# Optimization experiments

Measured on AMD Instinct MI355X. Metric: run time of the kernel, lower is better.

The kernel has to match this reference:

```python
import jax, jax.numpy as jnp
import numpy as np

B, S, D = 16, 1024, 768          # batch, seq_len, in_features
NS, MAXW = 256, 8                # num_spans, max span width (fixed for jit)
V, C = 128, 6                    # num_vertexes, max corefs per vertex
R = 512                          # num_max_rels_per_example
REL, HID, DIS = 97, 384, 20      # relation_num, hidden_dim, dis_size
NEG = -1e30


def setup_inputs() -> dict:
    key = jax.random.key(0)
    ks = jax.random.split(key, 14)
    sentence_repr = jax.random.normal(ks[0], (B, S, D), jnp.float32)
    starts = jax.random.randint(ks[1], (B, NS), 0, S - MAXW)
    widths = jax.random.randint(ks[2], (B, NS), 0, MAXW)
    entity_span_indices = jnp.stack([starts, starts + widths], axis=-1)  # (B,NS,2), start<=end
    entity_span_indices_mask = jax.random.randint(ks[3], (B, NS), 0, 2)
    vertex_indices = jax.random.randint(ks[4], (B, V, C), 0, NS)
    vertex_indices_mask = jax.random.randint(ks[5], (B, V, C), 0, 2)
    head_tail_indices = jax.random.randint(ks[6], (B, R, 2), 0, V)
    relation_mask = jax.random.randint(ks[7], (B, R), 0, 2)
    dis_h_2_t = jax.random.randint(ks[8], (B, R), 0, 20)
    dis_t_2_h = jax.random.randint(ks[9], (B, R), 0, 20)
    dis_embed = jax.random.normal(ks[10], (20, DIS), jnp.float32) * 0.02
    dis_embed = dis_embed.at[10].set(0.0)  # padding_idx=10
    fin = D + DIS                      # final_in_features with distance
    in_proj = 2 * fin + D              # concat [head+dis, tail+dis, head*tail]
    W1 = jax.random.normal(ks[11], (in_proj, HID), jnp.float32) / np.float32(np.sqrt(in_proj))
    W2 = jax.random.normal(ks[12], (HID, REL), jnp.float32) / np.float32(np.sqrt(HID))
    b2 = jnp.zeros((REL,), jnp.float32)
    return dict(sentence_repr=sentence_repr, entity_span_indices=entity_span_indices,
                entity_span_indices_mask=entity_span_indices_mask,
                vertex_indices=vertex_indices, vertex_indices_mask=vertex_indices_mask,
                head_tail_indices=head_tail_indices, relation_mask=relation_mask,
                dis_h_2_t=dis_h_2_t, dis_t_2_h=dis_t_2_h,
                dis_embed=dis_embed, W1=W1, W2=W2, b2=b2)


def reference(sentence_repr, entity_span_indices, entity_span_indices_mask,
              vertex_indices, vertex_indices_mask, head_tail_indices,
              relation_mask, dis_h_2_t, dis_t_2_h, dis_embed, W1, W2, b2):
    Bx, Sx, Dx = sentence_repr.shape
    # --- SpanExtractor: masked max pooling over tokens in each span [start, end] ---
    starts = entity_span_indices[..., 0]
    ends = entity_span_indices[..., 1]
    pos = starts[..., None] + jnp.arange(MAXW)            # (B,NS,W)
    valid = pos <= ends[..., None]
    posc = jnp.clip(pos, 0, Sx - 1).reshape(Bx, -1)       # (B,NS*W)
    tok = jnp.take_along_axis(sentence_repr, posc[..., None], axis=1)
    tok = tok.reshape(Bx, NS, MAXW, Dx)
    span_emb = jnp.where(valid[..., None], tok, NEG).max(axis=2)   # (B,NS,D)
    # --- coref 'mean' pooling over spans per vertex (batched_index_select) ---
    vidx = vertex_indices.reshape(Bx, -1)
    ve = jnp.take_along_axis(span_emb, vidx[..., None], axis=1).reshape(Bx, V, C, Dx)
    m = vertex_indices_mask.astype(jnp.float32)
    cnt = jnp.maximum(m.sum(axis=2), 1.0)                 # num_corefs clamped >=1
    vertex_emb = (ve * m[..., None]).sum(axis=2) / cnt[..., None]  # (B,V,D)
    # --- head/tail gather ---
    hti = head_tail_indices.reshape(Bx, -1)
    ht = jnp.take_along_axis(vertex_emb, hti[..., None], axis=1).reshape(Bx, R, 2, Dx)
    head_repr = ht[:, :, 0, :]
    tail_repr = ht[:, :, 1, :]
    # (original multiplies by relation_mask and discards the result -> no-op)
    eh = dis_embed[dis_h_2_t]                              # (B,R,DIS)
    et = dis_embed[dis_t_2_h]
    feat = jnp.concatenate([head_repr, eh, tail_repr, et, head_repr * tail_repr], axis=-1)
    # TwoLayerLinear: relu(x @ W1) @ W2 + b2, bias=(False, True)
    predict_re = jax.nn.relu(feat @ W1) @ W2 + b2          # (B,R,REL)
    return predict_re
```

## Files before the change

### kernel.cpp

```cpp
#include <hip/hip_runtime.h>
#include <cstdint>
#include <cstddef>

#define B_    16
#define S_    1024
#define D_    768
#define NS_   256
#define V_    128
#define C_    6
#define R_    512
#define REL_  97
#define HID_  384
#define DIS_  20
#define KD_   768
#define N2P_  128

typedef unsigned short ushort_t;
typedef unsigned int   u32;
typedef short bf16x4 __attribute__((ext_vector_type(4)));
typedef short bf16x8 __attribute__((ext_vector_type(8)));
typedef float f32x4  __attribute__((ext_vector_type(4)));
typedef float f32x16 __attribute__((ext_vector_type(16)));

__device__ __forceinline__ float bf2f(short s) {
    return __uint_as_float(((unsigned int)(unsigned short)s) << 16);
}
__device__ __forceinline__ short f2bf(float x) {
    union { float f; unsigned int u; } c; c.f = x;
    unsigned int r = (c.u + 0x7fffu + ((c.u >> 16) & 1u)) >> 16;
    return (short)(unsigned short)r;
}

typedef const __attribute__((address_space(1))) u32* gas_t;
typedef __attribute__((address_space(3))) u32*       las_t;
__device__ __forceinline__ void dma16(const void* g, void* l) {
    __builtin_amdgcn_global_load_lds((gas_t)g, (las_t)l, 16, 0, 0);
}

__global__ __launch_bounds__(192) void prep_kernel(
    const float* __restrict__ sr, const int* __restrict__ spans,
    const float* __restrict__ W1, const float* __restrict__ W2,
    const float* __restrict__ dis,
    ushort_t* __restrict__ span_emb, ushort_t* __restrict__ W1HT,
    ushort_t* __restrict__ W1P, ushort_t* __restrict__ W2T,
    float* __restrict__ disH, float* __restrict__ disT)
{
    int blk = blockIdx.x;
    int tid = threadIdx.x;
    if (blk < 4096) {
        int bn    = blk;
        int b     = bn >> 8;
        int start = spans[2 * bn];
        int end   = spans[2 * bn + 1];
        int w     = end - start;
        const float* base = sr + ((size_t)b * S_ + start) * D_ + tid * 4;
        f32x4 x[8];
        x[0] = *(const f32x4*)base;
        switch (w) {
        case 7: x[7] = *(const f32x4*)(base + 7 * D_); [[fallthrough]];
        case 6: x[6] = *(const f32x4*)(base + 6 * D_); [[fallthrough]];
        case 5: x[5] = *(const f32x4*)(base + 5 * D_); [[fallthrough]];
        case 4: x[4] = *(const f32x4*)(base + 4 * D_); [[fallthrough]];
        case 3: x[3] = *(const f32x4*)(base + 3 * D_); [[fallthrough]];
        case 2: x[2] = *(const f32x4*)(base + 2 * D_); [[fallthrough]];
        case 1: x[1] = *(const f32x4*)(base + 1 * D_); break;
        default: break;
        }
        f32x4 m = x[0];
#pragma unroll
        for (int j = 1; j < 8; ++j)
            if (j <= w) {
#pragma unroll
                for (int c = 0; c < 4; ++c) m[c] = fmaxf(m[c], x[j][c]);
            }
        bf16x4 o;
#pragma unroll
        for (int c = 0; c < 4; ++c) o[c] = f2bf(m[c]);
        *(bf16x4*)(span_emb + (size_t)bn * D_ + tid * 4) = o;
    } else if (blk < 4480) {
        int flat = (blk - 4096) * 192 + tid;
        int nn   = flat & 63;
        int kg   = (flat >> 6) & 7;
        int itnt = flat >> 9;
        int it   = itnt / 12;
        int nt   = itnt - it * 12;
        bf16x8 p;
#pragma unroll
        for (int j = 0; j < 8; ++j) {
            int k = it * 64 + kg * 8 + j;
            int n = nt * 64 + nn;
            float v = (n < HID_) ? W1[(size_t)k * HID_ + n]
                                 : W1[(size_t)(788 + k) * HID_ + (n - HID_)];
            p[j] = f2bf(v);
        }
        *(bf16x8*)(W1HT + ((size_t)itnt * 8 + kg) * 512 + nn * 8) = p;
    } else if (blk < 4672) {
        int flat = (blk - 4480) * 192 + tid;
        int nn   = flat & 63;
        int kg   = (flat >> 6) & 7;
        int itnt = flat >> 9;
        int it   = itnt / 6;
        int nt   = itnt - it * 6;
        bf16x8 p;
#pragma unroll
        for (int j = 0; j < 8; ++j) {
            int k = it * 64 + kg * 8 + j;
            int n = nt * 64 + nn;
            p[j] = f2bf(W1[(size_t)(1576 + k) * HID_ + n]);
        }
        *(bf16x8*)(W1P + ((size_t)itnt * 8 + kg) * 512 + nn * 8) = p;
    } else if (blk < 4704) {
        int g  = (blk - 4672) * 192 + tid;
        int n  = g / 48;
        int k0 = (g - n * 48) * 8;
        bf16x8 p;
#pragma unroll
        for (int j = 0; j < 8; ++j) {
            float v = (n < REL_) ? W2[(size_t)(k0 + j) * REL_ + n] : 0.f;
            p[j] = f2bf(v);
        }
        *(bf16x8*)(W2T + (size_t)n * HID_ + k0) = p;
    } else {
        int g   = (blk - 4704) * 192 + tid;
        int sel = g >= 7680;
        int gg  = sel ? g - 7680 : g;
        int i   = gg / HID_;
        int n   = gg - i * HID_;
        int rb  = sel ? 1556 : 768;
        float a = 0.f;
#pragma unroll
        for (int j = 0; j < DIS_; ++j)
            a += dis[i * DIS_ + j] * W1[(size_t)(rb + j) * HID_ + n];
        (sel ? disT : disH)[i * HID_ + n] = a;
    }
}

__global__ __launch_bounds__(192) void vertex_kernel(
    const ushort_t* __restrict__ span_emb, const int* __restrict__ vidx,
    const int* __restrict__ vmask, ushort_t* __restrict__ vembB)
{
    int bv = blockIdx.x;
    int b  = bv >> 7;
    const int* vi = vidx  + bv * C_;
    const int* vm = vmask + bv * C_;
    int   idxs[C_];
    float ms[C_];
    float cnt = 0.f;
#pragma unroll
    for (int c = 0; c < C_; ++c) {
        idxs[c] = vi[c];
        ms[c]   = (float)vm[c];
        cnt    += ms[c];
    }
    float inv = 1.f / fmaxf(cnt, 1.f);
    int col = threadIdx.x * 4;
    float s[4] = {0.f, 0.f, 0.f, 0.f};
#pragma unroll
    for (int c = 0; c < C_; ++c) {
        if (ms[c] != 0.f) {
            bf16x4 x = *(const bf16x4*)(span_emb +
                        ((size_t)(b * NS_ + idxs[c])) * D_ + col);
#pragma unroll
            for (int q = 0; q < 4; ++q) s[q] += bf2f(x[q]);
        }
    }
    bf16x4 o;
#pragma unroll
    for (int q = 0; q < 4; ++q) o[q] = f2bf(s[q] * inv);
    *(bf16x4*)(vembB + (size_t)bv * D_ + col) = o;
}

__global__ __launch_bounds__(256, 3) void gemmc_kernel(
    const ushort_t* __restrict__ vembB, const ushort_t* __restrict__ W1HT,
    float* __restrict__ vproj)
{
    __shared__ ushort_t Abuf[2][64][64];
    __shared__ ushort_t Bbuf[2][8][64][8];

    int tid  = threadIdx.x;
    int wv   = tid >> 6;
    int lane = tid & 63;
    int m0   = blockIdx.x * 64;
    int nt   = blockIdx.y;
    int n0   = nt * 64;

    int rr  = lane >> 3;
    int sl  = lane & 7;
    int gsw = (sl - rr) & 7;

    const ushort_t* asrc[2];
#pragma unroll
    for (int gi = 0; gi < 2; ++gi)
        asrc[gi] = vembB + (size_t)(m0 + wv * 16 + gi * 8 + rr) * KD_ + gsw * 8;

    auto stage = [&](int bf, int it) {
#pragma unroll
        for (int gi = 0; gi < 2; ++gi)
            dma16(asrc[gi] + it * 64, &Abuf[bf][wv * 16 + gi * 8][0]);
        const ushort_t* bbase = W1HT + ((size_t)it * 12 + nt) * 4096;
#pragma unroll
        for (int q = 0; q < 2; ++q) {
            int p = wv * 2 + q;
            dma16(bbase + (size_t)p * 512 + lane * 8, &Bbuf[bf][p][0][0]);
        }
    };

    int half = lane >> 5;
    int lrow = lane & 31;
    int wm   = (wv & 1) * 32;
    int wn   = (wv >> 1) * 32;

    f32x16 acc;
#pragma unroll
    for (int r = 0; r < 16; ++r) acc[r] = 0.f;

    stage(0, 0);
    for (int it = 0; it < 12; ++it) {
        int bf = it & 1;
        __syncthreads();
        if (it + 1 < 12) stage(bf ^ 1, it + 1);
#pragma unroll
        for (int s = 0; s < 4; ++s) {
            int kg   = s * 2 + half;
            int slot = ((kg + lrow) & 7) * 8;
            bf16x8 a = *(bf16x8*)&Abuf[bf][wm + lrow][slot];
            bf16x8 b = *(bf16x8*)&Bbuf[bf][kg][wn + lrow][0];
            acc = __builtin_amdgcn_mfma_f32_32x32x16_bf16(a, b, acc, 0, 0, 0);
        }
    }

    int col = n0 + wn + lrow;
#pragma unroll
    for (int r = 0; r < 16; ++r) {
        int row = m0 + wm + (r & 3) + 8 * (r >> 2) + 4 * half;
        vproj[(size_t)row * KD_ + col] = acc[r];
    }
}

__global__ __launch_bounds__(256, 3) void gemmd_kernel(
    const ushort_t* __restrict__ vembB, const int* __restrict__ ht,
    const int* __restrict__ dht, const int* __restrict__ dth,
    const ushort_t* __restrict__ W1P, const float* __restrict__ vproj,
    const float* __restrict__ disH, const float* __restrict__ disT,
    ushort_t* __restrict__ hidden)
{
    __shared__ ushort_t Abuf[2][64][64];
    __shared__ ushort_t Bbuf[2][8][64][8];
    __shared__ int hI[64], tI[64], dhI[64], dtI[64];

    int tid  = threadIdx.x;
    int wv   = tid >> 6;
    int lane = tid & 63;
    int m0   = blockIdx.x * 64;
    int nt   = blockIdx.y;
    int n0   = nt * 64;

    int rr  = lane >> 3;
    int sl  = lane & 7;
    int gsw = (sl - rr) & 7;

    if (tid < 64) {
        int g = m0 + tid;
        int b = g >> 9;
        hI[tid]  = b * V_ + ht[2 * g];
        tI[tid]  = b * V_ + ht[2 * g + 1];
        dhI[tid] = dht[g];
        dtI[tid] = dth[g];
    }

    int hoff[2], toff[2];
#pragma unroll
    for (int gi = 0; gi < 2; ++gi) {
        int g = m0 + wv * 16 + gi * 8 + rr;
        int b = g >> 9;
        hoff[gi] = (b * V_ + ht[2 * g])     * KD_;
        toff[gi] = (b * V_ + ht[2 * g + 1]) * KD_;
    }

    auto stage = [&](int bf, int it) {
        int kk = it * 64 + gsw * 8;
#pragma unroll
        for (int gi = 0; gi < 2; ++gi) {
            bf16x8 h = *(const bf16x8*)(vembB + hoff[gi] + kk);
            bf16x8 t = *(const bf16x8*)(vembB + toff[gi] + kk);
            bf16x8 p;
#pragma unroll
            for (int j = 0; j < 8; ++j) p[j] = f2bf(bf2f(h[j]) * bf2f(t[j]));
            *(bf16x8*)&Abuf[bf][wv * 16 + gi * 8 + rr][sl * 8] = p;
        }
        const ushort_t* bbase = W1P + ((size_t)it * 6 + nt) * 4096;
#pragma unroll
        for (int q = 0; q < 2; ++q) {
            int p = wv * 2 + q;
            dma16(bbase + (size_t)p * 512 + lane * 8, &Bbuf[bf][p][0][0]);
        }
    };

    int half = lane >> 5;
    int lrow = lane & 31;
    int wm   = (wv & 1) * 32;
    int wn   = (wv >> 1) * 32;

    f32x16 acc;
#pragma unroll
    for (int r = 0; r < 16; ++r) acc[r] = 0.f;

    stage(0, 0);
    for (int it = 0; it < 12; ++it) {
        int bf = it & 1;
        __syncthreads();
        if (it + 1 < 12) stage(bf ^ 1, it + 1);
#pragma unroll
        for (int s = 0; s < 4; ++s) {
            int kg   = s * 2 + half;
            int slot = ((kg + lrow) & 7) * 8;
            bf16x8 a = *(bf16x8*)&Abuf[bf][wm + lrow][slot];
            bf16x8 b = *(bf16x8*)&Bbuf[bf][kg][wn + lrow][0];
            acc = __builtin_amdgcn_mfma_f32_32x32x16_bf16(a, b, acc, 0, 0, 0);
        }
    }

    int col = n0 + wn + lrow;
#pragma unroll
    for (int r = 0; r < 16; ++r) {
        int rl = wm + (r & 3) + 8 * (r >> 2) + 4 * half;
        float v = acc[r]
                + vproj[(size_t)hI[rl] * KD_ + col]
                + vproj[(size_t)tI[rl] * KD_ + HID_ + col]
                + disH[dhI[rl] * HID_ + col]
                + disT[dtI[rl] * HID_ + col];
        hidden[(size_t)(m0 + rl) * HID_ + col] = (ushort_t)f2bf(fmaxf(v, 0.f));
    }
}

__global__ __launch_bounds__(256) void gemm2_kernel(
    const ushort_t* __restrict__ hidden, const ushort_t* __restrict__ W2T,
    const float* __restrict__ b2, float* __restrict__ out)
{
    __shared__ ushort_t As[32][72];
    __shared__ ushort_t Bs[128][72];

    int m0  = blockIdx.x * 32;
    int tid = threadIdx.x;

    int arow = tid >> 3;
    int akk  = (tid & 7) * 8;

    bf16x8 pA; bf16x8 pB[4];
    auto loadAB = [&](int k0) {
        pA = *(const bf16x8*)(hidden + (size_t)(m0 + arow) * HID_ + k0 + akk);
#pragma unroll
        for (int e = 0; e < 4; ++e)
            pB[e] = *(const bf16x8*)(W2T + (size_t)(arow + e * 32) * HID_ + k0 + akk);
    };

    int w    = tid >> 6;
    int lane = tid & 63;
    int wm = (w & 1) * 16;
    int wn = (w >> 1) * 64;
    int lr = lane & 15, lq = lane >> 4;

    f32x4 acc[4];
#pragma unroll
    for (int e = 0; e < 4; ++e) acc[e] = (f32x4){0.f, 0.f, 0.f, 0.f};

    loadAB(0);
    for (int k0 = 0; k0 < HID_; k0 += 64) {
        __syncthreads();
        *(bf16x8*)&As[arow][akk] = pA;
#pragma unroll
        for (int e = 0; e < 4; ++e)
            *(bf16x8*)&Bs[arow + e * 32][akk] = pB[e];
        __syncthreads();
        if (k0 + 64 < HID_) loadAB(k0 + 64);
#pragma unroll
        for (int ks = 0; ks < 2; ++ks) {
            int kb = ks * 32 + lq * 8;
            bf16x8 a = *(bf16x8*)&As[wm + lr][kb];
#pragma unroll
            for (int nf = 0; nf < 4; ++nf) {
                bf16x8 bb = *(bf16x8*)&Bs[wn + nf * 16 + lr][kb];
                acc[nf] = __builtin_amdgcn_mfma_f32_16x16x32_bf16(a, bb, acc[nf], 0, 0, 0);
            }
        }
    }

    int grow = m0 + wm + lq * 4;
#pragma unroll
    for (int nf = 0; nf < 4; ++nf) {
        int col = wn + nf * 16 + lr;
        if (col < REL_) {
            float bias = b2[col];
#pragma unroll
            for (int r = 0; r < 4; ++r)
                out[(size_t)(grow + r) * REL_ + col] = acc[nf][r] + bias;
        }
    }
}

extern "C" void kernel_launch(void* const* d_in, const int* in_sizes, int n_in,
                              void* d_out, int out_size, void* d_ws, size_t ws_size,
                              hipStream_t stream)
{
    const float* sr    = (const float*)d_in[0];
    const int*   spans = (const int*)  d_in[1];
    const int*   vidx  = (const int*)  d_in[3];
    const int*   vmask = (const int*)  d_in[4];
    const int*   ht    = (const int*)  d_in[5];
    const int*   dht   = (const int*)  d_in[7];
    const int*   dth   = (const int*)  d_in[8];
    const float* dis   = (const float*)d_in[9];
    const float* W1    = (const float*)d_in[10];
    const float* W2    = (const float*)d_in[11];
    const float* b2    = (const float*)d_in[12];
    float* out = (float*)d_out;

    ushort_t* span_emb = (ushort_t*)d_ws;
    ushort_t* vembB    = span_emb + (size_t)B_ * NS_ * D_;
    ushort_t* W1HT     = vembB + (size_t)B_ * V_ * D_;
    ushort_t* W1P      = W1HT + (size_t)144 * 4096;
    ushort_t* W2T      = W1P + (size_t)72 * 4096;
    ushort_t* hidden   = W2T + (size_t)N2P_ * HID_;
    float* vproj = (float*)(hidden + (size_t)B_ * R_ * HID_);
    float* disH  = vproj + (size_t)B_ * V_ * KD_;
    float* disT  = disH + (size_t)DIS_ * HID_;

    prep_kernel<<<4784, 192, 0, stream>>>(
        sr, spans, W1, W2, dis, span_emb, W1HT, W1P, W2T, disH, disT);
    vertex_kernel<<<B_ * V_, 192, 0, stream>>>(span_emb, vidx, vmask, vembB);

    gemmc_kernel<<<dim3(32, 12), 256, 0, stream>>>(vembB, W1HT, vproj);
    gemmd_kernel<<<dim3(128, 6), 256, 0, stream>>>(
        vembB, ht, dht, dth, W1P, vproj, disH, disT, hidden);

    gemm2_kernel<<<(B_ * R_) / 32, 256, 0, stream>>>(hidden, W2T, b2, out);
}
```

Baseline: 151.6 us.

## Fuse all five stages into one cooperative persistent kernel with grid syncs

Replaces the five separate launches (prep, vertex pooling, two first-layer GEMMs, second GEMM) with one cooperative kernel. The stages are separated by grid.sync() and their work is distributed with grid-stride loops. The aim is to remove per-launch overhead and the drain and fill gaps between kernels. In exchange it needs cooperative launch, caps occupancy via launch bounds, and keeps the old multi-kernel path as a fallback when the stream is being captured or the cooperative launch fails.

```diff
diff --git a/kernel.cpp b/kernel.cpp
--- a/kernel.cpp
+++ b/kernel.cpp
@@ -1,6 +1,9 @@
 #include <hip/hip_runtime.h>
+#include <hip/hip_cooperative_groups.h>
 #include <cstdint>
 #include <cstddef>
+
+namespace cg = cooperative_groups;
 
 #define B_    16
 #define S_    1024
@@ -14,6 +17,8 @@
 #define DIS_  20
 #define KD_   768
 #define N2P_  128
+#define NBLK  768
+#define NTHR  256
 
 typedef unsigned short ushort_t;
 typedef unsigned int   u32;
@@ -35,6 +40,347 @@
 typedef __attribute__((address_space(3))) u32*       las_t;
 __device__ __forceinline__ void dma16(const void* g, void* l) {
     __builtin_amdgcn_global_load_lds((gas_t)g, (las_t)l, 16, 0, 0);
+}
+
+__global__ __launch_bounds__(NTHR, 3) void mega_kernel(
+    const float* __restrict__ sr, const int* __restrict__ spans,
+    const int* __restrict__ vidx, const int* __restrict__ vmask,
+    const int* __restrict__ ht, const int* __restrict__ dht,
+    const int* __restrict__ dth, const float* __restrict__ dis,
+    const float* __restrict__ W1, const float* __restrict__ W2,
+    const float* __restrict__ b2,
+    ushort_t* __restrict__ span_emb, ushort_t* __restrict__ vembB,
+    ushort_t* __restrict__ W1HT, ushort_t* __restrict__ W1P,
+    ushort_t* __restrict__ W2T, float* __restrict__ disH,
+    float* __restrict__ disT, ushort_t* __restrict__ hidden,
+    float* __restrict__ vproj, float* __restrict__ out)
+{
+    cg::grid_group grid = cg::this_grid();
+
+    __shared__ union {
+        struct {
+            ushort_t A[2][64][64];
+            ushort_t Bp[2][8][64][8];
+            int hI[64], tI[64], dhI[64], dtI[64];
+        } cd;
+        struct {
+            ushort_t As[32][72];
+            ushort_t Bs[128][72];
+        } g2;
+    } sm;
+
+    const int tid   = threadIdx.x;
+    const int blk   = blockIdx.x;
+    const int lane  = tid & 63;
+    const int wv    = tid >> 6;
+    const int nblks = gridDim.x;
+    const int gtid  = blk * NTHR + tid;
+    const int nthrd = nblks * NTHR;
+
+    {
+        const int waveid = blk * 4 + wv;
+        const int nwaves = nblks * 4;
+        for (int task = waveid; task < 12288; task += nwaves) {
+            int bn = task & 4095;
+            int q  = task >> 12;
+            int b  = bn >> 8;
+            int start = spans[2 * bn];
+            int end   = spans[2 * bn + 1];
+            int w     = end - start;
+            int col   = q * 256 + lane * 4;
+            const float* base = sr + ((size_t)b * S_ + start) * D_ + col;
+            f32x4 x[8];
+            x[0] = *(const f32x4*)base;
+            switch (w) {
+            case 7: x[7] = *(const f32x4*)(base + 7 * D_); [[fallthrough]];
+            case 6: x[6] = *(const f32x4*)(base + 6 * D_); [[fallthrough]];
+            case 5: x[5] = *(const f32x4*)(base + 5 * D_); [[fallthrough]];
+            case 4: x[4] = *(const f32x4*)(base + 4 * D_); [[fallthrough]];
+            case 3: x[3] = *(const f32x4*)(base + 3 * D_); [[fallthrough]];
+            case 2: x[2] = *(const f32x4*)(base + 2 * D_); [[fallthrough]];
+            case 1: x[1] = *(const f32x4*)(base + 1 * D_); break;
+            default: break;
+            }
+            f32x4 m = x[0];
+#pragma unroll
+            for (int j = 1; j < 8; ++j)
+                if (j <= w) {
+#pragma unroll
+                    for (int c = 0; c < 4; ++c) m[c] = fmaxf(m[c], x[j][c]);
+                }
+            bf16x4 o;
+#pragma unroll
+            for (int c = 0; c < 4; ++c) o[c] = f2bf(m[c]);
+            *(bf16x4*)(span_emb + (size_t)bn * D_ + col) = o;
+        }
+    }
+    for (int g0 = gtid; g0 < 132096; g0 += nthrd) {
+        if (g0 < 73728) {
+            int g = g0;
+            int nn = g & 63, kg = (g >> 6) & 7, itnt = g >> 9;
+            int it = itnt / 12, nt = itnt - it * 12;
+            bf16x8 p;
+#pragma unroll
+            for (int j = 0; j < 8; ++j) {
+                int k = it * 64 + kg * 8 + j;
+                int n = nt * 64 + nn;
+                float v = (n < HID_) ? W1[(size_t)k * HID_ + n]
+                                     : W1[(size_t)(788 + k) * HID_ + (n - HID_)];
+                p[j] = f2bf(v);
+            }
+            *(bf16x8*)(W1HT + ((size_t)itnt * 8 + kg) * 512 + nn * 8) = p;
+        } else if (g0 < 110592) {
+            int g = g0 - 73728;
+            int nn = g & 63, kg = (g >> 6) & 7, itnt = g >> 9;
+            int it = itnt / 6, nt = itnt - it * 6;
+            bf16x8 p;
+#pragma unroll
+            for (int j = 0; j < 8; ++j) {
+                int k = it * 64 + kg * 8 + j;
+                int n = nt * 64 + nn;
+                p[j] = f2bf(W1[(size_t)(1576 + k) * HID_ + n]);
+            }
+            *(bf16x8*)(W1P + ((size_t)itnt * 8 + kg) * 512 + nn * 8) = p;
+        } else if (g0 < 116736) {
+            int g = g0 - 110592;
+            int n = g / 48, k0 = (g - n * 48) * 8;
+            bf16x8 p;
+#pragma unroll
+            for (int j = 0; j < 8; ++j) {
+                float v = (n < REL_) ? W2[(size_t)(k0 + j) * REL_ + n] : 0.f;
+                p[j] = f2bf(v);
+            }
+            *(bf16x8*)(W2T + (size_t)n * HID_ + k0) = p;
+        } else {
+            int g = g0 - 116736;
+            int sel = g >= 7680;
+            int gg = sel ? g - 7680 : g;
+            int i = gg / HID_, n = gg - (gg / HID_) * HID_;
+            int rb = sel ? 1556 : 768;
+            float a = 0.f;
+#pragma unroll
+            for (int j = 0; j < DIS_; ++j)
+                a += dis[i * DIS_ + j] * W1[(size_t)(rb + j) * HID_ + n];
+            (sel ? disT : disH)[i * HID_ + n] = a;
+        }
+    }
+
+    grid.sync();
+
+    for (int task = gtid; task < 393216; task += nthrd) {
+        int bv  = task / 192;
+        int grp = task - bv * 192;
+        int b   = bv >> 7;
+        const int* vi = vidx  + bv * C_;
+        const int* vm = vmask + bv * C_;
+        float cnt = 0.f;
+        float sacc[4] = {0.f, 0.f, 0.f, 0.f};
+        int col = grp * 4;
+#pragma unroll
+        for (int c = 0; c < C_; ++c) {
+            int mc = vm[c];
+            cnt += (float)mc;
+            if (mc) {
+                bf16x4 x = *(const bf16x4*)(span_emb +
+                            ((size_t)(b * NS_ + vi[c])) * D_ + col);
+#pragma unroll
+                for (int q = 0; q < 4; ++q) sacc[q] += bf2f(x[q]);
+            }
+        }
+        float inv = 1.f / fmaxf(cnt, 1.f);
+        bf16x4 o;
+#pragma unroll
+        for (int q = 0; q < 4; ++q) o[q] = f2bf(sacc[q] * inv);
+        *(bf16x4*)(vembB + (size_t)bv * D_ + col) = o;
+    }
+
+    grid.sync();
+
+    for (int bt = blk; bt < 384; bt += nblks) {
+        const int mb = bt & 31, nt = bt >> 5;
+        const int m0 = mb * 64, n0 = nt * 64;
+        const int rr = lane >> 3, sl = lane & 7;
+        const int gsw = (sl - rr) & 7;
+
+        const ushort_t* asrc0 = vembB + (size_t)(m0 + wv * 16 + rr) * KD_ + gsw * 8;
+        const ushort_t* asrc1 = asrc0 + 8 * KD_;
+
+        auto stageC = [&](int bf, int it) {
+            dma16(asrc0 + it * 64, &sm.cd.A[bf][wv * 16][0]);
+            dma16(asrc1 + it * 64, &sm.cd.A[bf][wv * 16 + 8][0]);
+            const ushort_t* bbase = W1HT + ((size_t)it * 12 + nt) * 4096;
+#pragma unroll
+            for (int q = 0; q < 2; ++q) {
+                int p = wv * 2 + q;
+                dma16(bbase + (size_t)p * 512 + lane * 8, &sm.cd.Bp[bf][p][0][0]);
+            }
+        };
+
+        const int half = lane >> 5, lrow = lane & 31;
+        const int wm = (wv & 1) * 32, wn = (wv >> 1) * 32;
+
+        f32x16 acc;
+#pragma unroll
+        for (int r = 0; r < 16; ++r) acc[r] = 0.f;
+
+        stageC(0, 0);
+        for (int it = 0; it < 12; ++it) {
+            int bf = it & 1;
+            __syncthreads();
+            if (it + 1 < 12) stageC(bf ^ 1, it + 1);
+#pragma unroll
+            for (int s = 0; s < 4; ++s) {
+                int kg   = s * 2 + half;
+                int slot = ((kg + lrow) & 7) * 8;
+                bf16x8 a = *(bf16x8*)&sm.cd.A[bf][wm + lrow][slot];
+                bf16x8 b = *(bf16x8*)&sm.cd.Bp[bf][kg][wn + lrow][0];
+                acc = __builtin_amdgcn_mfma_f32_32x32x16_bf16(a, b, acc, 0, 0, 0);
+            }
+        }
+        int col = n0 + wn + lrow;
+#pragma unroll
+        for (int r = 0; r < 16; ++r) {
+            int row = m0 + wm + (r & 3) + 8 * (r >> 2) + 4 * half;
+            vproj[(size_t)row * KD_ + col] = acc[r];
+        }
+    }
+
+    grid.sync();
+
+    for (int bt = blk; bt < 768; bt += nblks) {
+        __syncthreads();
+        const int mb = bt & 127, nt = bt >> 7;
+        const int m0 = mb * 64, n0 = nt * 64;
+        const int rr = lane >> 3, sl = lane & 7;
+        const int gsw = (sl - rr) & 7;
+
+        if (tid < 64) {
+            int g = m0 + tid;
+            int b = g >> 9;
+            sm.cd.hI[tid]  = b * V_ + ht[2 * g];
+            sm.cd.tI[tid]  = b * V_ + ht[2 * g + 1];
+            sm.cd.dhI[tid] = dht[g];
+            sm.cd.dtI[tid] = dth[g];
+        }
+
+        int hoff[2], toff[2];
+#pragma unroll
+        for (int gi = 0; gi < 2; ++gi) {
+            int g = m0 + wv * 16 + gi * 8 + rr;
+            int b = g >> 9;
+            hoff[gi] = (b * V_ + ht[2 * g])     * KD_;
+            toff[gi] = (b * V_ + ht[2 * g + 1]) * KD_;
+        }
+
+        auto stageD = [&](int bf, int it) {
+            int kk = it * 64 + gsw * 8;
+#pragma unroll
+            for (int gi = 0; gi < 2; ++gi) {
+                bf16x8 h = *(const bf16x8*)(vembB + hoff[gi] + kk);
+                bf16x8 t = *(const bf16x8*)(vembB + toff[gi] + kk);
+                bf16x8 p;
+#pragma unroll
+                for (int j = 0; j < 8; ++j) p[j] = f2bf(bf2f(h[j]) * bf2f(t[j]));
+                *(bf16x8*)&sm.cd.A[bf][wv * 16 + gi * 8 + rr][sl * 8] = p;
+            }
+            const ushort_t* bbase = W1P + ((size_t)it * 6 + nt) * 4096;
+#pragma unroll
+            for (int q = 0; q < 2; ++q) {
+                int p = wv * 2 + q;
+                dma16(bbase + (size_t)p * 512 + lane * 8, &sm.cd.Bp[bf][p][0][0]);
+            }
+        };
+
+        const int half = lane >> 5, lrow = lane & 31;
+        const int wm = (wv & 1) * 32, wn = (wv >> 1) * 32;
+
+        f32x16 acc;
+#pragma unroll
+        for (int r = 0; r < 16; ++r) acc[r] = 0.f;
+
+        stageD(0, 0);
+        for (int it = 0; it < 12; ++it) {
+            int bf = it & 1;
+            __syncthreads();
+            if (it + 1 < 12) stageD(bf ^ 1, it + 1);
+#pragma unroll
+            for (int s = 0; s < 4; ++s) {
+                int kg   = s * 2 + half;
+                int slot = ((kg + lrow) & 7) * 8;
+                bf16x8 a = *(bf16x8*)&sm.cd.A[bf][wm + lrow][slot];
+                bf16x8 b = *(bf16x8*)&sm.cd.Bp[bf][kg][wn + lrow][0];
+                acc = __builtin_amdgcn_mfma_f32_32x32x16_bf16(a, b, acc, 0, 0, 0);
+            }
+        }
+
+        int col = n0 + wn + lrow;
+#pragma unroll
+        for (int r = 0; r < 16; ++r) {
+            int rl = wm + (r & 3) + 8 * (r >> 2) + 4 * half;
+            float v = acc[r]
+                    + vproj[(size_t)sm.cd.hI[rl] * KD_ + col]
+                    + vproj[(size_t)sm.cd.tI[rl] * KD_ + HID_ + col]
+                    + disH[sm.cd.dhI[rl] * HID_ + col]
+                    + disT[sm.cd.dtI[rl] * HID_ + col];
+            hidden[(size_t)(m0 + rl) * HID_ + col] = (ushort_t)f2bf(fmaxf(v, 0.f));
+        }
+    }
+
+    grid.sync();
+
+    for (int bt = blk; bt < 256; bt += nblks) {
+        const int m0 = bt * 32;
+        const int arow = tid >> 3;
+        const int akk  = (tid & 7) * 8;
+
+        bf16x8 pA; bf16x8 pB[4];
+        auto loadAB = [&](int k0) {
+            pA = *(const bf16x8*)(hidden + (size_t)(m0 + arow) * HID_ + k0 + akk);
+#pragma unroll
+            for (int e = 0; e < 4; ++e)
+                pB[e] = *(const bf16x8*)(W2T + (size_t)(arow + e * 32) * HID_ + k0 + akk);
+        };
+
+        const int wm = (wv & 1) * 16, wn = (wv >> 1) * 64;
+        const int lr = lane & 15, lq = lane >> 4;
+
+        f32x4 acc[4];
+#pragma unroll
+        for (int e = 0; e < 4; ++e) acc[e] = (f32x4){0.f, 0.f, 0.f, 0.f};
+
+        loadAB(0);
+        for (int k0 = 0; k0 < HID_; k0 += 64) {
+            __syncthreads();
+            *(bf16x8*)&sm.g2.As[arow][akk] = pA;
+#pragma unroll
+            for (int e = 0; e < 4; ++e)
+                *(bf16x8*)&sm.g2.Bs[arow + e * 32][akk] = pB[e];
+            __syncthreads();
+            if (k0 + 64 < HID_) loadAB(k0 + 64);
+#pragma unroll
+            for (int ks = 0; ks < 2; ++ks) {
+                int kb = ks * 32 + lq * 8;
+                bf16x8 a = *(bf16x8*)&sm.g2.As[wm + lr][kb];
+#pragma unroll
+                for (int nf = 0; nf < 4; ++nf) {
+                    bf16x8 bb = *(bf16x8*)&sm.g2.Bs[wn + nf * 16 + lr][kb];
+                    acc[nf] = __builtin_amdgcn_mfma_f32_16x16x32_bf16(a, bb, acc[nf], 0, 0, 0);
+                }
+            }
+        }
+
+        int grow = m0 + wm + lq * 4;
+#pragma unroll
+        for (int nf = 0; nf < 4; ++nf) {
+            int col = wn + nf * 16 + lr;
+            if (col < REL_) {
+                float bias = b2[col];
+#pragma unroll
+                for (int r = 0; r < 4; ++r)
+                    out[(size_t)(grow + r) * REL_ + col] = acc[nf][r] + bias;
+            }
+        }
+    }
 }
 
 __global__ __launch_bounds__(192) void prep_kernel(
@@ -425,13 +771,41 @@
     float* disH  = vproj + (size_t)B_ * V_ * KD_;
     float* disT  = disH + (size_t)DIS_ * HID_;
 
-    prep_kernel<<<4784, 192, 0, stream>>>(
-        sr, spans, W1, W2, dis, span_emb, W1HT, W1P, W2T, disH, disT);
-    vertex_kernel<<<B_ * V_, 192, 0, stream>>>(span_emb, vidx, vmask, vembB);
-
-    gemmc_kernel<<<dim3(32, 12), 256, 0, stream>>>(vembB, W1HT, vproj);
-    gemmd_kernel<<<dim3(128, 6), 256, 0, stream>>>(
-        vembB, ht, dht, dth, W1P, vproj, disH, disT, hidden);
-
-    gemm2_kernel<<<(B_ * R_) / 32, 256, 0, stream>>>(hidden, W2T, b2, out);
-}
+    bool done = false;
+    hipStreamCaptureStatus cs = hipStreamCaptureStatusNone;
+    if (hipStreamIsCapturing(stream, &cs) != hipSuccess)
+        cs = hipStreamCaptureStatusActive;
+    if (cs == hipStreamCaptureStatusNone) {
+        int maxB = 0;
+        if (hipOccupancyMaxActiveBlocksPerMultiprocessor(&maxB, mega_kernel,
+                                                         NTHR, 0) == hipSuccess
+            && maxB >= 1) {
+            int nblk = 256 * maxB;
+            if (nblk > NBLK) nblk = NBLK;
+            void* args[] = {
+                (void*)&sr, (void*)&spans, (void*)&vidx, (void*)&vmask,
+                (void*)&ht, (void*)&dht, (void*)&dth, (void*)&dis,
+                (void*)&W1, (void*)&W2, (void*)&b2,
+                (void*)&span_emb, (void*)&vembB, (void*)&W1HT, (void*)&W1P,
+                (void*)&W2T, (void*)&disH, (void*)&disT, (void*)&hidden,
+                (void*)&vproj, (void*)&out
+            };
+            if (hipLaunchCooperativeKernel((void*)mega_kernel, dim3(nblk),
+                                           dim3(NTHR), args, 0, stream)
+                == hipSuccess)
+                done = true;
+            else
+                (void)hipGetLastError();
+        }
+    }
+
+    if (!done) {
+        prep_kernel<<<4784, 192, 0, stream>>>(
+            sr, spans, W1, W2, dis, span_emb, W1HT, W1P, W2T, disH, disT);
+        vertex_kernel<<<B_ * V_, 192, 0, stream>>>(span_emb, vidx, vmask, vembB);
+        gemmc_kernel<<<dim3(32, 12), 256, 0, stream>>>(vembB, W1HT, vproj);
+        gemmd_kernel<<<dim3(128, 6), 256, 0, stream>>>(
+            vembB, ht, dht, dth, W1P, vproj, disH, disT, hidden);
+        gemm2_kernel<<<(B_ * R_) / 32, 256, 0, stream>>>(hidden, W2T, b2, out);
+    }
+}
```

Result: no change. 149.9 us (-1.1%).

## Fuse span max-pooling into vertex mean kernel, drop span_emb buffer

Applied to the files above, without the earlier changes.

The separate span-embedding pass and vertex pooling kernel are merged. Each vertex block now recomputes the max-pool of its masked coref spans directly from the fp32 sentence representation and averages them, with no bf16 span_emb intermediate and one fewer launch. The grid shrinks from 4096 span blocks to 2048 vertex blocks. In exchange, spans referenced by several vertices are recomputed and fp32 rows are re-read per coref (up to 6 per vertex, about half masked), which can raise global reads compared with computing each span once.

```diff
diff --git a/kernel.cpp b/kernel.cpp
--- a/kernel.cpp
+++ b/kernel.cpp
@@ -37,48 +37,65 @@
     __builtin_amdgcn_global_load_lds((gas_t)g, (las_t)l, 16, 0, 0);
 }
 
-__global__ __launch_bounds__(192) void prep_kernel(
+__global__ __launch_bounds__(192) void fused_prep_kernel(
     const float* __restrict__ sr, const int* __restrict__ spans,
+    const int* __restrict__ vidx, const int* __restrict__ vmask,
     const float* __restrict__ W1, const float* __restrict__ W2,
     const float* __restrict__ dis,
-    ushort_t* __restrict__ span_emb, ushort_t* __restrict__ W1HT,
+    ushort_t* __restrict__ vembB, ushort_t* __restrict__ W1HT,
     ushort_t* __restrict__ W1P, ushort_t* __restrict__ W2T,
     float* __restrict__ disH, float* __restrict__ disT)
 {
     int blk = blockIdx.x;
     int tid = threadIdx.x;
-    if (blk < 4096) {
-        int bn    = blk;
-        int b     = bn >> 8;
-        int start = spans[2 * bn];
-        int end   = spans[2 * bn + 1];
-        int w     = end - start;
-        const float* base = sr + ((size_t)b * S_ + start) * D_ + tid * 4;
-        f32x4 x[8];
-        x[0] = *(const f32x4*)base;
-        switch (w) {
-        case 7: x[7] = *(const f32x4*)(base + 7 * D_); [[fallthrough]];
-        case 6: x[6] = *(const f32x4*)(base + 6 * D_); [[fallthrough]];
-        case 5: x[5] = *(const f32x4*)(base + 5 * D_); [[fallthrough]];
-        case 4: x[4] = *(const f32x4*)(base + 4 * D_); [[fallthrough]];
-        case 3: x[3] = *(const f32x4*)(base + 3 * D_); [[fallthrough]];
-        case 2: x[2] = *(const f32x4*)(base + 2 * D_); [[fallthrough]];
-        case 1: x[1] = *(const f32x4*)(base + 1 * D_); break;
-        default: break;
-        }
-        f32x4 m = x[0];
-#pragma unroll
-        for (int j = 1; j < 8; ++j)
-            if (j <= w) {
-#pragma unroll
-                for (int c = 0; c < 4; ++c) m[c] = fmaxf(m[c], x[j][c]);
+    if (blk < 2048) {
+        int bv = blk;
+        int b  = bv >> 7;
+        const int* vi = vidx  + bv * C_;
+        const int* vm = vmask + bv * C_;
+        int col = tid * 4;
+        float s[4] = {0.f, 0.f, 0.f, 0.f};
+        float cnt = 0.f;
+#pragma unroll
+        for (int c = 0; c < C_; ++c) {
+            int mc = vm[c];
+            cnt += (float)mc;
+            if (mc) {
+                int sn    = b * NS_ + vi[c];
+                int start = spans[2 * sn];
+                int end   = spans[2 * sn + 1];
+                int w     = end - start;
+                const float* base = sr + ((size_t)b * S_ + start) * D_ + col;
+                f32x4 x[8];
+                x[0] = *(const f32x4*)base;
+                switch (w) {
+                case 7: x[7] = *(const f32x4*)(base + 7 * D_); [[fallthrough]];
+                case 6: x[6] = *(const f32x4*)(base + 6 * D_); [[fallthrough]];
+                case 5: x[5] = *(const f32x4*)(base + 5 * D_); [[fallthrough]];
+                case 4: x[4] = *(const f32x4*)(base + 4 * D_); [[fallthrough]];
+                case 3: x[3] = *(const f32x4*)(base + 3 * D_); [[fallthrough]];
+                case 2: x[2] = *(const f32x4*)(base + 2 * D_); [[fallthrough]];
+                case 1: x[1] = *(const f32x4*)(base + 1 * D_); break;
+                default: break;
+                }
+                f32x4 m = x[0];
+#pragma unroll
+                for (int j = 1; j < 8; ++j)
+                    if (j <= w) {
+#pragma unroll
+                        for (int q = 0; q < 4; ++q) m[q] = fmaxf(m[q], x[j][q]);
+                    }
+#pragma unroll
+                for (int q = 0; q < 4; ++q) s[q] += bf2f(f2bf(m[q]));
             }
+        }
+        float inv = 1.f / fmaxf(cnt, 1.f);
         bf16x4 o;
 #pragma unroll
-        for (int c = 0; c < 4; ++c) o[c] = f2bf(m[c]);
-        *(bf16x4*)(span_emb + (size_t)bn * D_ + tid * 4) = o;
-    } else if (blk < 4480) {
-        int flat = (blk - 4096) * 192 + tid;
+        for (int q = 0; q < 4; ++q) o[q] = f2bf(s[q] * inv);
+        *(bf16x4*)(vembB + (size_t)bv * D_ + col) = o;
+    } else if (blk < 2432) {
+        int flat = (blk - 2048) * 192 + tid;
         int nn   = flat & 63;
         int kg   = (flat >> 6) & 7;
         int itnt = flat >> 9;
@@ -94,8 +111,8 @@
             p[j] = f2bf(v);
         }
         *(bf16x8*)(W1HT + ((size_t)itnt * 8 + kg) * 512 + nn * 8) = p;
-    } else if (blk < 4672) {
-        int flat = (blk - 4480) * 192 + tid;
+    } else if (blk < 2624) {
+        int flat = (blk - 2432) * 192 + tid;
         int nn   = flat & 63;
         int kg   = (flat >> 6) & 7;
         int itnt = flat >> 9;
@@ -109,8 +126,8 @@
             p[j] = f2bf(W1[(size_t)(1576 + k) * HID_ + n]);
         }
         *(bf16x8*)(W1P + ((size_t)itnt * 8 + kg) * 512 + nn * 8) = p;
-    } else if (blk < 4704) {
-        int g  = (blk - 4672) * 192 + tid;
+    } else if (blk < 2656) {
+        int g  = (blk - 2624) * 192 + tid;
         int n  = g / 48;
         int k0 = (g - n * 48) * 8;
         bf16x8 p;
@@ -121,7 +138,7 @@
         }
         *(bf16x8*)(W2T + (size_t)n * HID_ + k0) = p;
     } else {
-        int g   = (blk - 4704) * 192 + tid;
+        int g   = (blk - 2656) * 192 + tid;
         int sel = g >= 7680;
         int gg  = sel ? g - 7680 : g;
         int i   = gg / HID_;
@@ -133,41 +150,6 @@
             a += dis[i * DIS_ + j] * W1[(size_t)(rb + j) * HID_ + n];
         (sel ? disT : disH)[i * HID_ + n] = a;
     }
-}
-
-__global__ __launch_bounds__(192) void vertex_kernel(
-    const ushort_t* __restrict__ span_emb, const int* __restrict__ vidx,
-    const int* __restrict__ vmask, ushort_t* __restrict__ vembB)
-{
-    int bv = blockIdx.x;
-    int b  = bv >> 7;
-    const int* vi = vidx  + bv * C_;
-    const int* vm = vmask + bv * C_;
-    int   idxs[C_];
-    float ms[C_];
-    float cnt = 0.f;
-#pragma unroll
-    for (int c = 0; c < C_; ++c) {
-        idxs[c] = vi[c];
-        ms[c]   = (float)vm[c];
-        cnt    += ms[c];
-    }
-    float inv = 1.f / fmaxf(cnt, 1.f);
-    int col = threadIdx.x * 4;
-    float s[4] = {0.f, 0.f, 0.f, 0.f};
-#pragma unroll
-    for (int c = 0; c < C_; ++c) {
-        if (ms[c] != 0.f) {
-            bf16x4 x = *(const bf16x4*)(span_emb +
-                        ((size_t)(b * NS_ + idxs[c])) * D_ + col);
-#pragma unroll
-            for (int q = 0; q < 4; ++q) s[q] += bf2f(x[q]);
-        }
-    }
-    bf16x4 o;
-#pragma unroll
-    for (int q = 0; q < 4; ++q) o[q] = f2bf(s[q] * inv);
-    *(bf16x4*)(vembB + (size_t)bv * D_ + col) = o;
 }
 
 __global__ __launch_bounds__(256, 3) void gemmc_kernel(
@@ -415,23 +397,20 @@
     const float* b2    = (const float*)d_in[12];
     float* out = (float*)d_out;
 
-    ushort_t* span_emb = (ushort_t*)d_ws;
-    ushort_t* vembB    = span_emb + (size_t)B_ * NS_ * D_;
-    ushort_t* W1HT     = vembB + (size_t)B_ * V_ * D_;
-    ushort_t* W1P      = W1HT + (size_t)144 * 4096;
-    ushort_t* W2T      = W1P + (size_t)72 * 4096;
-    ushort_t* hidden   = W2T + (size_t)N2P_ * HID_;
+    ushort_t* vembB  = (ushort_t*)d_ws;
+    ushort_t* W1HT   = vembB + (size_t)B_ * V_ * D_;
+    ushort_t* W1P    = W1HT + (size_t)144 * 4096;
+    ushort_t* W2T    = W1P + (size_t)72 * 4096;
+    ushort_t* hidden = W2T + (size_t)N2P_ * HID_;
     float* vproj = (float*)(hidden + (size_t)B_ * R_ * HID_);
     float* disH  = vproj + (size_t)B_ * V_ * KD_;
     float* disT  = disH + (size_t)DIS_ * HID_;
 
-    prep_kernel<<<4784, 192, 0, stream>>>(
-        sr, spans, W1, W2, dis, span_emb, W1HT, W1P, W2T, disH, disT);
-    vertex_kernel<<<B_ * V_, 192, 0, stream>>>(span_emb, vidx, vmask, vembB);
-
+    fused_prep_kernel<<<2736, 192, 0, stream>>>(
+        sr, spans, vidx, vmask, W1, W2, dis,
+        vembB, W1HT, W1P, W2T, disH, disT);
     gemmc_kernel<<<dim3(32, 12), 256, 0, stream>>>(vembB, W1HT, vproj);
     gemmd_kernel<<<dim3(128, 6), 256, 0, stream>>>(
         vembB, ht, dht, dth, W1P, vproj, disH, disT, hidden);
-
     gemm2_kernel<<<(B_ * R_) / 32, 256, 0, stream>>>(hidden, W2T, b2, out);
 }
```

New measurement: 158.4 us. 4.5% more time.
